# Performance work log

Measured on AMD Instinct MI355X. Metric: run time of the kernel, lower is better.

Reference implementation:

```python
import math
import jax, jax.numpy as jnp
import numpy as np

DIM = 2048
NUM_HEADS = 32
NUM_KV_HEADS = 8
HEAD_DIM = DIM // NUM_HEADS
KV_REPEAT = NUM_HEADS // NUM_KV_HEADS
BSZ, SEQ = 2, 2048
THRESHOLD = 0.05


def ternarize_ste(w):
    # scale = mean(|w|), clamped; ternary in {-1,0,1}; STE: fwd value is ternary,
    # grad flows straight through to w.
    scale = jnp.maximum(jnp.abs(w).mean(), 1e-6)
    ternary = jnp.where(w > THRESHOLD * scale, 1.0,
                        jnp.where(w < -THRESHOLD * scale, -1.0, 0.0)).astype(w.dtype)
    return w + jax.lax.stop_gradient(ternary - w)


def setup_inputs() -> dict:
    key = jax.random.key(0)
    kx, kq, kk, kv, ko = jax.random.split(key, 5)
    # kaiming_uniform_(a=sqrt(5)) => U(-b, b) with b = 1/sqrt(in_features)
    bound = 1.0 / math.sqrt(DIM)
    return {
        "x": jax.random.normal(kx, (BSZ, SEQ, DIM), dtype=jnp.float32),
        "wq": jax.random.uniform(kq, (DIM, DIM), jnp.float32, -bound, bound),
        "wk": jax.random.uniform(kk, (HEAD_DIM * NUM_KV_HEADS, DIM), jnp.float32, -bound, bound),
        "wv": jax.random.uniform(kv, (HEAD_DIM * NUM_KV_HEADS, DIM), jnp.float32, -bound, bound),
        "wo": jax.random.uniform(ko, (DIM, DIM), jnp.float32, -bound, bound),
    }


def reference(x, wq, wk, wv, wo):
    bsz, seq, _ = x.shape
    # BitLinear projections with ternarized weights (F.linear: x @ W^T)
    q = x @ ternarize_ste(wq).T                      # [b, s, dim]
    k = x @ ternarize_ste(wk).T                      # [b, s, kvh*hd]
    v = x @ ternarize_ste(wv).T

    q = q.reshape(bsz, seq, NUM_HEADS, HEAD_DIM)     # [b, s, H, d]
    k = k.reshape(bsz, seq, NUM_KV_HEADS, HEAD_DIM)
    v = v.reshape(bsz, seq, NUM_KV_HEADS, HEAD_DIM)
    # repeat_interleave over the kv-head axis to match query heads
    k = jnp.repeat(k, KV_REPEAT, axis=2)             # [b, s, H, d]
    v = jnp.repeat(v, KV_REPEAT, axis=2)

    scale = 1.0 / math.sqrt(HEAD_DIM)
    att = jnp.einsum('bqhd,bkhd->bhqk', q, k) * scale  # [b, H, s, s]
    causal = jnp.tril(jnp.ones((seq, seq), dtype=bool))
    att = jnp.where(causal, att, -jnp.inf)
    probs = jax.nn.softmax(att, axis=-1)
    out = jnp.einsum('bhqk,bkhd->bqhd', probs, v).reshape(bsz, seq, DIM)
    return out @ ternarize_ste(wo).T
```

## Files before the change

### kernel.cpp

```cpp
#include <hip/hip_runtime.h>

typedef _Float16 f16;
typedef f16  f16x8 __attribute__((ext_vector_type(8)));
typedef f16  f16x4 __attribute__((ext_vector_type(4)));
typedef float f32x4 __attribute__((ext_vector_type(4)));

#define DIM_   2048
#define SEQ_   2048
#define BATCH_ 2
#define MROWS_ (BATCH_*SEQ_)
#define HD_    64
#define KVW_   512

__device__ __forceinline__ f32x4 mfma16(f16x8 a, f16x8 b, f32x4 c) {
  return __builtin_amdgcn_mfma_f32_16x16x32_f16(a, b, c, 0, 0, 0);
}

typedef const __attribute__((address_space(1))) void gas_void;
typedef __attribute__((address_space(3))) void las_void;
__device__ __forceinline__ void gload16(const void* g, void* l) {
  __builtin_amdgcn_global_load_lds((gas_void*)g, (las_void*)l, 16, 0, 0);
}

__device__ __forceinline__ unsigned long long pk4(float a, float b, float c, float d) {
  union { _Float16 h[4]; unsigned long long u; } z;
  auto p0 = __builtin_amdgcn_cvt_pkrtz(a, b);
  auto p1 = __builtin_amdgcn_cvt_pkrtz(c, d);
  z.h[0] = p0[0]; z.h[1] = p0[1]; z.h[2] = p1[0]; z.h[3] = p1[1];
  return z.u;
}

__global__ __launch_bounds__(256)
void prep1(const float* __restrict__ x,
           const float* __restrict__ w0, const float* __restrict__ w1,
           const float* __restrict__ w2, const float* __restrict__ w3,
           float* __restrict__ parts, f16* __restrict__ hi, f16* __restrict__ lo) {
  const int id = blockIdx.y;
  if (id < 4) {
    const float* w = id == 0 ? w0 : id == 1 ? w1 : id == 2 ? w2 : w3;
    const int n4 = (id == 1 || id == 2) ? (KVW_ * DIM_ / 4) : (DIM_ * DIM_ / 4);
    float s = 0.f;
    for (int i = blockIdx.x * 256 + threadIdx.x; i < n4; i += gridDim.x * 256) {
      float4 v = *(const float4*)(w + (long)i * 4);
      s += fabsf(v.x) + fabsf(v.y) + fabsf(v.z) + fabsf(v.w);
    }
    #pragma unroll
    for (int off = 32; off > 0; off >>= 1)
      s += __shfl_down(s, off, 64);
    __shared__ float red[4];
    int lane = threadIdx.x & 63, wv = threadIdx.x >> 6;
    if (lane == 0) red[wv] = s;
    __syncthreads();
    if (threadIdx.x == 0)
      parts[id * 192 + blockIdx.x] = (red[0] + red[1]) + (red[2] + red[3]);
  } else {
    const int half = (MROWS_ * DIM_ / 4) / 2;
    const long base = (long)(id - 4) * half;
    for (int i = blockIdx.x * 256 + threadIdx.x; i < half; i += gridDim.x * 256) {
      float4 v = *(const float4*)(x + (base + i) * 4);
      f16x4 h, l;
      h[0] = (f16)v.x; l[0] = (f16)(v.x - (float)h[0]);
      h[1] = (f16)v.y; l[1] = (f16)(v.y - (float)h[1]);
      h[2] = (f16)v.z; l[2] = (f16)(v.z - (float)h[2]);
      h[3] = (f16)v.w; l[3] = (f16)(v.w - (float)h[3]);
      *(f16x4*)(hi + (base + i) * 4) = h;
      *(f16x4*)(lo + (base + i) * 4) = l;
    }
  }
}

__global__ __launch_bounds__(256)
void ternarize4(const float* __restrict__ w0, const float* __restrict__ w1,
                const float* __restrict__ w2, const float* __restrict__ w3,
                unsigned short* __restrict__ t0, unsigned short* __restrict__ t1,
                unsigned short* __restrict__ t2, unsigned short* __restrict__ t3,
                const float* __restrict__ parts) {
  const int id = blockIdx.y;
  const float* w = id == 0 ? w0 : id == 1 ? w1 : id == 2 ? w2 : w3;
  unsigned short* t = id == 0 ? t0 : id == 1 ? t1 : id == 2 ? t2 : t3;
  const int n = (id == 1 || id == 2) ? (KVW_ * DIM_) : (DIM_ * DIM_);

  __shared__ float thr_s;
  if (threadIdx.x < 64) {
    const int lane = threadIdx.x;
    float s = parts[id * 192 + lane] + parts[id * 192 + 64 + lane]
            + parts[id * 192 + 128 + lane];
    #pragma unroll
    for (int off = 32; off > 0; off >>= 1)
      s += __shfl_down(s, off, 64);
    if (lane == 0) thr_s = 0.05f * fmaxf(s / (float)n, 1e-6f);
  }
  __syncthreads();
  const float thr = thr_s;

  const int n4 = n >> 2;
  for (int i = blockIdx.x * 256 + threadIdx.x; i < n4; i += gridDim.x * 256) {
    float4 v = *(const float4*)(w + (long)i * 4);
    ushort4 o;
    o.x = v.x > thr ? 0x3C00 : (v.x < -thr ? 0xBC00 : 0);
    o.y = v.y > thr ? 0x3C00 : (v.y < -thr ? 0xBC00 : 0);
    o.z = v.z > thr ? 0x3C00 : (v.z < -thr ? 0xBC00 : 0);
    o.w = v.w > thr ? 0x3C00 : (v.w < -thr ? 0xBC00 : 0);
    *(ushort4*)(t + (long)i * 4) = o;
  }
}

__global__ __launch_bounds__(256, 2)
void gemm_qkv(const f16* __restrict__ Ah, const f16* __restrict__ Al,
              const f16* __restrict__ Bw,
              f16* __restrict__ O1, f16* __restrict__ O2,
              f16* __restrict__ K1, f16* __restrict__ K2,
              f16* __restrict__ OV) {
  constexpr int BUFSZ = 32768;
  __shared__ __attribute__((aligned(16))) char smem[2 * BUFSZ];

  const int id2 = (blockIdx.x & 7) * 48 + (blockIdx.x >> 3);
  const int bx  = id2 % 12;
  const int by  = id2 / 12;
  const int brow = by * 128;
  const int bcol = bx * 256;

  const int tid  = threadIdx.x;
  const int lane = tid & 63;
  const int wv   = tid >> 6;
  const int wr   = (wv >> 1) * 64;
  const int wc   = (wv & 1) * 128;
  const int fr   = lane & 15;
  const int fq   = lane >> 4;

  const bool lo_on = bcol < 2560;

  const int rl  = lane >> 2;
  const int scg = ((lane & 3) ^ ((lane >> 3) & 3)) * 8;
  const f16* gA0 = Ah + (long)(brow + wv * 32 + rl) * DIM_ + scg;
  const f16* gL0 = Al + (long)(brow + wv * 32 + rl) * DIM_ + scg;
  const f16* gB0 = Bw + (long)(bcol + wv * 64 + rl) * DIM_ + scg;
  const int wvbA = __builtin_amdgcn_readfirstlane(wv * 1024);
  const int wvbB = __builtin_amdgcn_readfirstlane(wv * 2048);

  auto STAGE = [&](int kt, int buf) {
    const int k0 = kt * 32;
    char* base = smem + buf * BUFSZ;
    f16* lA = (f16*)base + wvbA;
    f16* lL = (f16*)(base + 8192) + wvbA;
    f16* lB = (f16*)(base + 16384) + wvbB;
    gload16(gA0 + k0, lA);
    gload16(gA0 + k0 + 16 * DIM_, lA + 512);
    gload16(gB0 + k0, lB);
    gload16(gB0 + k0 + 16 * DIM_, lB + 512);
    gload16(gB0 + k0 + 32 * DIM_, lB + 1024);
    gload16(gB0 + k0 + 48 * DIM_, lB + 1536);
    if (lo_on) {
      gload16(gL0 + k0, lL);
      gload16(gL0 + k0 + 16 * DIM_, lL + 512);
    }
  };

  const int xga = (fq ^ ((fr >> 1) & 3)) * 8;

  f32x4 acc[4][8] = {};
  const int nk = DIM_ / 32;

  STAGE(0, 0);
  #pragma unroll 1
  for (int kt = 0; kt < nk; ++kt) {
    asm volatile("s_waitcnt vmcnt(0)" ::: "memory");
    __syncthreads();
    if (kt + 1 < nk) STAGE(kt + 1, (kt + 1) & 1);

    const char* base = smem + (kt & 1) * BUFSZ;
    const f16* cAh = (const f16*)base;
    const f16* cAl = (const f16*)(base + 8192);
    const f16* cB  = (const f16*)(base + 16384);

    f16x8 bfr[8];
    #pragma unroll
    for (int ni = 0; ni < 8; ++ni)
      bfr[ni] = *(const f16x8*)(cB + (wc + ni * 16 + fr) * 32 + xga);
    #pragma unroll
    for (int mi = 0; mi < 4; ++mi) {
      const int aoff = (wr + mi * 16 + fr) * 32 + xga;
      f16x8 ah = *(const f16x8*)(cAh + aoff);
      #pragma unroll
      for (int ni = 0; ni < 8; ++ni)
        acc[mi][ni] = mfma16(ah, bfr[ni], acc[mi][ni]);
      if (lo_on) {
        f16x8 al = *(const f16x8*)(cAl + aoff);
        #pragma unroll
        for (int ni = 0; ni < 8; ++ni)
          acc[mi][ni] = mfma16(al, bfr[ni], acc[mi][ni]);
      }
    }
  }

  const int colbase = bcol + wc;
  if (colbase < 2048) {
    #pragma unroll
    for (int mi = 0; mi < 4; ++mi)
      #pragma unroll
      for (int ni = 0; ni < 8; ++ni)
        #pragma unroll
        for (int r = 0; r < 4; ++r) {
          long idx = (long)(brow + wr + mi * 16 + fq * 4 + r) * DIM_
                   + colbase + ni * 16 + fr;
          float v = acc[mi][ni][r];
          f16 hv = (f16)v;
          O1[idx] = hv;
          O2[idx] = (f16)(v - (float)hv);
        }
  } else if (colbase < 2560) {
    #pragma unroll
    for (int mi = 0; mi < 4; ++mi)
      #pragma unroll
      for (int ni = 0; ni < 8; ++ni)
        #pragma unroll
        for (int r = 0; r < 4; ++r) {
          long idx = (long)(brow + wr + mi * 16 + fq * 4 + r) * KVW_
                   + (colbase - 2048) + ni * 16 + fr;
          float v = acc[mi][ni][r];
          f16 hv = (f16)v;
          K1[idx] = hv;
          K2[idx] = (f16)(v - (float)hv);
        }
  } else {
    f16* st = (f16*)smem + wv * 32 * 72;
    const int bb = brow >> 11;
    const int s0 = (brow & (SEQ_ - 1)) + wr;
    #pragma unroll
    for (int nh = 0; nh < 4; ++nh) {
      const int khh = ((colbase - 2560) >> 6) + (nh >> 1);
      const int db  = (nh & 1) * 32;
      #pragma unroll
      for (int nj = 0; nj < 2; ++nj) {
        const int ni = nh * 2 + nj;
        #pragma unroll
        for (int mi = 0; mi < 4; ++mi)
          #pragma unroll
          for (int r = 0; r < 4; ++r)
            st[(nj * 16 + fr) * 72 + mi * 16 + fq * 4 + r] = (f16)acc[mi][ni][r];
      }
      #pragma unroll
      for (int i = 0; i < 4; ++i) {
        int dl = i * 8 + (lane >> 3);
        f16x8 v = *(const f16x8*)(st + dl * 72 + (lane & 7) * 8);
        *(f16x8*)(OV + ((long)(bb * 8 + khh) * 64 + db + dl) * SEQ_
                  + s0 + (lane & 7) * 8) = v;
      }
    }
  }
}

__global__ __launch_bounds__(256)
void gemm_o(const f16* __restrict__ A, const f16* __restrict__ Bw,
            float* __restrict__ C) {
  constexpr int BUFSZ = 16384;
  __shared__ __attribute__((aligned(16))) char smem[2 * BUFSZ];

  const int cpx = gridDim.x >> 3;
  const int id2 = (blockIdx.x & 7) * cpx + (blockIdx.x >> 3);
  const int nbx = DIM_ >> 7;
  const int bx  = id2 % nbx;
  const int by  = id2 / nbx;
  const int brow = by * 128;
  const int bcol = bx * 128;

  const int tid  = threadIdx.x;
  const int lane = tid & 63;
  const int wv   = tid >> 6;
  const int wr   = (wv >> 1) * 64;
  const int wc   = (wv & 1) * 64;
  const int fr   = lane & 15;
  const int fq   = lane >> 4;

  const int srw = wv * 32 + (lane >> 2);
  const int scg = ((lane & 3) ^ ((lane >> 3) & 3)) * 8;
  const f16* gA0 = A + (long)(brow + srw) * DIM_ + scg;
  const f16* gA1 = gA0 + 16 * (long)DIM_;
  const f16* gB0 = Bw + (long)(bcol + srw) * DIM_ + scg;
  const f16* gB1 = gB0 + 16 * (long)DIM_;
  const int wvb = __builtin_amdgcn_readfirstlane(wv * 1024);

  auto STAGE = [&](int kt, int buf) {
    const int k0 = kt * 32;
    char* base = smem + buf * BUFSZ;
    f16* lA = (f16*)base + wvb;
    f16* lB = (f16*)(base + 8192) + wvb;
    gload16(gA0 + k0, lA);
    gload16(gA1 + k0, lA + 512);
    gload16(gB0 + k0, lB);
    gload16(gB1 + k0, lB + 512);
  };

  const int xga = (fq ^ ((fr >> 1) & 3)) * 8;

  f32x4 acc[4][4] = {};
  const int nk = DIM_ >> 5;

  STAGE(0, 0);
  #pragma unroll 1
  for (int kt = 0; kt < nk; ++kt) {
    asm volatile("s_waitcnt vmcnt(0)" ::: "memory");
    __syncthreads();
    if (kt + 1 < nk) STAGE(kt + 1, (kt + 1) & 1);

    const char* base = smem + (kt & 1) * BUFSZ;
    const f16* cA = (const f16*)base;
    const f16* cB = (const f16*)(base + 8192);

    f16x8 bfr[4];
    #pragma unroll
    for (int ni = 0; ni < 4; ++ni)
      bfr[ni] = *(const f16x8*)(cB + (wc + ni * 16 + fr) * 32 + xga);
    #pragma unroll
    for (int mi = 0; mi < 4; ++mi) {
      f16x8 ah = *(const f16x8*)(cA + (wr + mi * 16 + fr) * 32 + xga);
      #pragma unroll
      for (int ni = 0; ni < 4; ++ni)
        acc[mi][ni] = mfma16(ah, bfr[ni], acc[mi][ni]);
    }
  }

  #pragma unroll
  for (int mi = 0; mi < 4; ++mi)
    #pragma unroll
    for (int ni = 0; ni < 4; ++ni)
      #pragma unroll
      for (int r = 0; r < 4; ++r)
        C[(long)(brow + wr + mi * 16 + fq * 4 + r) * DIM_ + (bcol + wc + ni * 16 + fr)]
            = acc[mi][ni][r];
}

__global__ __launch_bounds__(256, 2)
void attn_kernel(const f16* __restrict__ qhi, const f16* __restrict__ qlo,
                 const f16* __restrict__ khi, const f16* __restrict__ klo,
                 const f16* __restrict__ vt,  f16* __restrict__ AO) {
  const int id2  = (blockIdx.x & 7) * 64 + (blockIdx.x >> 3);
  const int pr   = id2 & 31;
  const int cmb  = id2 >> 5;
  const int kh   = cmb & 7;
  const int b    = cmb >> 3;
  const int tid  = threadIdx.x;
  const int lane = tid & 63;
  const int w    = tid >> 6;
  const int fr   = lane & 15;
  const int fq   = lane >> 4;
  const int h    = kh * 4 + w;
  const int xr   = (fr & 7) << 4;

  __shared__ __attribute__((aligned(16))) char sKh[2][64 * 128];
  __shared__ __attribute__((aligned(16))) char sKl[2][64 * 128];
  __shared__ __attribute__((aligned(16))) char sVt[2][64 * 128];
  __shared__ __attribute__((aligned(16))) char sP [4][2][16 * 128];

  const int srow = w * 16 + (lane >> 3);
  const int scol = ((lane & 7) ^ (lane >> 3)) * 8;
  const f16* gK0 = khi + ((long)(b * SEQ_) + srow) * KVW_ + kh * HD_ + scol;
  const f16* gL0 = klo + ((long)(b * SEQ_) + srow) * KVW_ + kh * HD_ + scol;
  const f16* gV0 = vt + ((long)(b * 8 + kh) * HD_ + srow) * SEQ_ + scol;
  const int ldso = __builtin_amdgcn_readfirstlane(w * 2048);

  auto STAGE = [&](int kb, int buf) {
    const long ko = (long)kb * 64 * KVW_;
    const long vo = (long)kb * 64;
    gload16(gK0 + ko,             (char*)sKh[buf] + ldso);
    gload16(gK0 + ko + 8 * KVW_,  (char*)sKh[buf] + ldso + 1024);
    gload16(gL0 + ko,             (char*)sKl[buf] + ldso);
    gload16(gL0 + ko + 8 * KVW_,  (char*)sKl[buf] + ldso + 1024);
    gload16(gV0 + vo,             (char*)sVt[buf] + ldso);
    gload16(gV0 + vo + 8 * SEQ_,  (char*)sVt[buf] + ldso + 1024);
  };

  char* pw0 = sP[w][0];
  char* pw1 = sP[w][1];
  const float ce = 0.125f * 1.44269504f;

  #pragma unroll 1
  for (int pass = 0; pass < 2; ++pass) {
    const int t     = pass ? (63 - pr) : pr;
    const int nkv   = (t >> 1) + 1;
    const int qrow0 = t * 32;

    f16x8 qh[2][2], ql[2][2];
    #pragma unroll
    for (int st = 0; st < 2; ++st)
      #pragma unroll
      for (int ks = 0; ks < 2; ++ks) {
        const long qoff = (long)(b * SEQ_ + qrow0 + st * 16 + fr) * DIM_
                        + h * HD_ + ks * 32 + fq * 8;
        qh[st][ks] = *(const f16x8*)(qhi + qoff);
        ql[st][ks] = *(const f16x8*)(qlo + qoff);
      }

    __syncthreads();
    STAGE(0, 0);

    float m0 = -1e30f, m1 = -1e30f, l0 = 0.f, l1 = 0.f;
    f32x4 o0[4] = {}, o1[4] = {};
    int c = 0;

    #pragma unroll 1
    for (int kb = 0; kb < nkv; ++kb) {
      asm volatile("s_waitcnt vmcnt(0)" ::: "memory");
      __syncthreads();
      if (kb + 1 < nkv) STAGE(kb + 1, c ^ 1);
      const char* bK = sKh[c]; const char* bL = sKl[c]; const char* bV = sVt[c];

      f32x4 s0[4] = {}, s1[4] = {};
      __builtin_amdgcn_s_setprio(1);
      #pragma unroll
      for (int ks = 0; ks < 2; ++ks)
        #pragma unroll
        for (int ni = 0; ni < 4; ++ni) {
          const int rb = (ni * 16 + fr) * 128 + ((ks * 64 + fq * 16) ^ xr);
          f16x8 ah = *(const f16x8*)(bK + rb);
          f16x8 af = *(const f16x8*)(bL + rb);
          s0[ni] = mfma16(ah, qh[0][ks], s0[ni]);
          s0[ni] = mfma16(ah, ql[0][ks], s0[ni]);
          s0[ni] = mfma16(af, qh[0][ks], s0[ni]);
          s1[ni] = mfma16(ah, qh[1][ks], s1[ni]);
          s1[ni] = mfma16(ah, ql[1][ks], s1[ni]);
          s1[ni] = mfma16(af, qh[1][ks], s1[ni]);
        }
      __builtin_amdgcn_s_setprio(0);
      if (kb == nkv - 1) {
        #pragma unroll
        for (int ni = 0; ni < 4; ++ni)
          #pragma unroll
          for (int r = 0; r < 4; ++r) {
            const int kk = ni * 16 + fq * 4 + r;
            if (kk > (t & 1) * 32 + fr)      s0[ni][r] = -1e30f;
            if (kk > (t & 1) * 32 + 16 + fr) s1[ni][r] = -1e30f;
          }
      }

      #pragma unroll
      for (int st = 0; st < 2; ++st) {
        f32x4* s = st ? s1 : s0;
        float& m = st ? m1 : m0;
        float& l = st ? l1 : l0;
        f32x4* o = st ? o1 : o0;
        char* pw = st ? pw1 : pw0;

        float ma = fmaxf(fmaxf(s[0][0], s[0][1]), fmaxf(s[0][2], s[0][3]));
        float mb2 = fmaxf(fmaxf(s[1][0], s[1][1]), fmaxf(s[1][2], s[1][3]));
        float mc = fmaxf(fmaxf(s[2][0], s[2][1]), fmaxf(s[2][2], s[2][3]));
        float md = fmaxf(fmaxf(s[3][0], s[3][1]), fmaxf(s[3][2], s[3][3]));
        float mb = fmaxf(fmaxf(ma, mb2), fmaxf(mc, md));
        mb = fmaxf(mb, __shfl_xor(mb, 16, 64));
        mb = fmaxf(mb, __shfl_xor(mb, 32, 64));

        const float mo = m;
        const bool trig = mb > mo + 64.f;
        const float mn = trig ? mb : mo;
        m = mn;
        const float al = exp2f((mo - mn) * ce);
        const float tt = mn * ce;

        float rs = 0.f;
        #pragma unroll
        for (int ni = 0; ni < 4; ++ni) {
          #pragma unroll
          for (int r = 0; r < 4; ++r) {
            float pv = exp2f(fmaf(s[ni][r], ce, -tt));
            s[ni][r] = pv;
            rs += pv;
          }
          *(unsigned long long*)(pw + ((fr * 128 + ni * 32 + fq * 8) ^ xr)) =
              pk4(s[ni][0], s[ni][1], s[ni][2], s[ni][3]);
        }
        rs += __shfl_xor(rs, 16, 64);
        rs += __shfl_xor(rs, 32, 64);
        l = l * al + rs;

        if (__any(trig)) {
          #pragma unroll
          for (int r = 0; r < 4; ++r) {
            float alr = __shfl(al, ((lane >> 4) << 2) + r, 64);
            o[0][r] *= alr; o[1][r] *= alr; o[2][r] *= alr; o[3][r] *= alr;
          }
        }
      }

      __builtin_amdgcn_s_setprio(1);
      #pragma unroll
      for (int ks = 0; ks < 2; ++ks) {
        const int pb = (fr * 128 + ks * 64 + fq * 16) ^ xr;
        f16x8 pa0 = *(const f16x8*)(pw0 + pb);
        f16x8 pa1 = *(const f16x8*)(pw1 + pb);
        #pragma unroll
        for (int di = 0; di < 4; ++di) {
          f16x8 vf = *(const f16x8*)(bV + (di * 16 + fr) * 128
                                     + ((ks * 64 + fq * 16) ^ xr));
          o0[di] = mfma16(pa0, vf, o0[di]);
          o1[di] = mfma16(pa1, vf, o1[di]);
        }
      }
      __builtin_amdgcn_s_setprio(0);
      c ^= 1;
    }

    #pragma unroll
    for (int st = 0; st < 2; ++st) {
      const f32x4* o = st ? o1 : o0;
      const float l = st ? l1 : l0;
      float linv[4];
      #pragma unroll
      for (int r = 0; r < 4; ++r)
        linv[r] = 1.f / __shfl(l, ((lane >> 4) << 2) + r, 64);
      #pragma unroll
      for (int di = 0; di < 4; ++di)
        #pragma unroll
        for (int r = 0; r < 4; ++r)
          AO[(long)(b * SEQ_ + qrow0 + st * 16 + fq * 4 + r) * DIM_
             + h * HD_ + di * 16 + fr] = (f16)(o[di][r] * linv[r]);
    }
  }
}

extern "C" void kernel_launch(void* const* d_in, const int* in_sizes, int n_in,
                              void* d_out, int out_size, void* d_ws, size_t ws_size,
                              hipStream_t stream) {
  const float* x  = (const float*)d_in[0];
  const float* wq = (const float*)d_in[1];
  const float* wk = (const float*)d_in[2];
  const float* wv = (const float*)d_in[3];
  const float* wo = (const float*)d_in[4];
  char* ws = (char*)d_ws;

  size_t off = 0;
  float* parts = (float*)ws;                off = 4096;
  f16* x_hi  = (f16*)(ws + off);            off += (size_t)MROWS_ * DIM_ * 2;
  f16* x_lo  = (f16*)(ws + off);            off += (size_t)MROWS_ * DIM_ * 2;
  f16* wq_t  = (f16*)(ws + off);            off += (size_t)DIM_ * DIM_ * 2;
  f16* wkv_t = (f16*)(ws + off);            off += (size_t)1024 * DIM_ * 2;
  f16* wo_t  = (f16*)(ws + off);            off += (size_t)DIM_ * DIM_ * 2;
  f16* qhi   = (f16*)(ws + off);            off += (size_t)MROWS_ * DIM_ * 2;
  f16* qlo   = (f16*)(ws + off);            off += (size_t)MROWS_ * DIM_ * 2;
  f16* khi   = (f16*)(ws + off);            off += (size_t)MROWS_ * KVW_ * 2;
  f16* klo   = (f16*)(ws + off);            off += (size_t)MROWS_ * KVW_ * 2;
  f16* vtb   = (f16*)(ws + off);            off += (size_t)BATCH_ * 8 * 64 * SEQ_ * 2;
  f16* ao    = (f16*)(ws + off);            off += (size_t)MROWS_ * DIM_ * 2;

  prep1<<<dim3(192, 6), dim3(256), 0, stream>>>(x, wq, wk, wv, wo,
                                                parts, x_hi, x_lo);
  ternarize4<<<dim3(192, 4), dim3(256), 0, stream>>>(
      wq, wk, wv, wo,
      (unsigned short*)wq_t, (unsigned short*)wkv_t,
      (unsigned short*)(wkv_t + (size_t)KVW_ * DIM_), (unsigned short*)wo_t,
      parts);

  gemm_qkv<<<dim3(384), dim3(256), 0, stream>>>(
      x_hi, x_lo, wq_t, qhi, qlo, khi, klo, vtb);

  attn_kernel<<<dim3(32 * 8 * BATCH_), dim3(256), 0, stream>>>(
      qhi, qlo, khi, klo, vtb, ao);

  gemm_o<<<dim3((DIM_ / 128) * (MROWS_ / 128)), dim3(256), 0, stream>>>(
      ao, wo_t, (float*)d_out);
}
```

Before: 284.6 us.

## Single-buffer K tiles in attention to fit three blocks per CU

```diff
diff --git a/kernel.cpp b/kernel.cpp
--- a/kernel.cpp
+++ b/kernel.cpp
@@ -330,7 +330,7 @@
             = acc[mi][ni][r];
 }
 
-__global__ __launch_bounds__(256, 2)
+__global__ __launch_bounds__(256, 3)
 void attn_kernel(const f16* __restrict__ qhi, const f16* __restrict__ qlo,
                  const f16* __restrict__ khi, const f16* __restrict__ klo,
                  const f16* __restrict__ vt,  f16* __restrict__ AO) {
@@ -347,8 +347,8 @@
   const int h    = kh * 4 + w;
   const int xr   = (fr & 7) << 4;
 
-  __shared__ __attribute__((aligned(16))) char sKh[2][64 * 128];
-  __shared__ __attribute__((aligned(16))) char sKl[2][64 * 128];
+  __shared__ __attribute__((aligned(16))) char sKh[64 * 128];
+  __shared__ __attribute__((aligned(16))) char sKl[64 * 128];
   __shared__ __attribute__((aligned(16))) char sVt[2][64 * 128];
   __shared__ __attribute__((aligned(16))) char sP [4][2][16 * 128];
 
@@ -359,15 +359,17 @@
   const f16* gV0 = vt + ((long)(b * 8 + kh) * HD_ + srow) * SEQ_ + scol;
   const int ldso = __builtin_amdgcn_readfirstlane(w * 2048);
 
-  auto STAGE = [&](int kb, int buf) {
+  auto STAGE_K = [&](int kb) {
     const long ko = (long)kb * 64 * KVW_;
+    gload16(gK0 + ko,            sKh + ldso);
+    gload16(gK0 + ko + 8 * KVW_, sKh + ldso + 1024);
+    gload16(gL0 + ko,            sKl + ldso);
+    gload16(gL0 + ko + 8 * KVW_, sKl + ldso + 1024);
+  };
+  auto STAGE_V = [&](int kb, int buf) {
     const long vo = (long)kb * 64;
-    gload16(gK0 + ko,             (char*)sKh[buf] + ldso);
-    gload16(gK0 + ko + 8 * KVW_,  (char*)sKh[buf] + ldso + 1024);
-    gload16(gL0 + ko,             (char*)sKl[buf] + ldso);
-    gload16(gL0 + ko + 8 * KVW_,  (char*)sKl[buf] + ldso + 1024);
-    gload16(gV0 + vo,             (char*)sVt[buf] + ldso);
-    gload16(gV0 + vo + 8 * SEQ_,  (char*)sVt[buf] + ldso + 1024);
+    gload16(gV0 + vo,            (char*)sVt[buf] + ldso);
+    gload16(gV0 + vo + 8 * SEQ_, (char*)sVt[buf] + ldso + 1024);
   };
 
   char* pw0 = sP[w][0];
@@ -392,18 +394,18 @@
       }
 
     __syncthreads();
-    STAGE(0, 0);
+    STAGE_K(0);
+    STAGE_V(0, 0);
 
     float m0 = -1e30f, m1 = -1e30f, l0 = 0.f, l1 = 0.f;
     f32x4 o0[4] = {}, o1[4] = {};
-    int c = 0;
 
     #pragma unroll 1
     for (int kb = 0; kb < nkv; ++kb) {
       asm volatile("s_waitcnt vmcnt(0)" ::: "memory");
       __syncthreads();
-      if (kb + 1 < nkv) STAGE(kb + 1, c ^ 1);
-      const char* bK = sKh[c]; const char* bL = sKl[c]; const char* bV = sVt[c];
+      if (kb + 1 < nkv) STAGE_V(kb + 1, (kb + 1) & 1);
+      const char* bV = sVt[kb & 1];
 
       f32x4 s0[4] = {}, s1[4] = {};
       __builtin_amdgcn_s_setprio(1);
@@ -412,8 +414,8 @@
         #pragma unroll
         for (int ni = 0; ni < 4; ++ni) {
           const int rb = (ni * 16 + fr) * 128 + ((ks * 64 + fq * 16) ^ xr);
-          f16x8 ah = *(const f16x8*)(bK + rb);
-          f16x8 af = *(const f16x8*)(bL + rb);
+          f16x8 ah = *(const f16x8*)(sKh + rb);
+          f16x8 af = *(const f16x8*)(sKl + rb);
           s0[ni] = mfma16(ah, qh[0][ks], s0[ni]);
           s0[ni] = mfma16(ah, ql[0][ks], s0[ni]);
           s0[ni] = mfma16(af, qh[0][ks], s0[ni]);
@@ -422,6 +424,10 @@
           s1[ni] = mfma16(af, qh[1][ks], s1[ni]);
         }
       __builtin_amdgcn_s_setprio(0);
+
+      __syncthreads();
+      if (kb + 1 < nkv) STAGE_K(kb + 1);
+
       if (kb == nkv - 1) {
         #pragma unroll
         for (int ni = 0; ni < 4; ++ni)
@@ -496,7 +502,6 @@
         }
       }
       __builtin_amdgcn_s_setprio(0);
-      c ^= 1;
     }
 
     #pragma unroll
```

New measurement: 284.7 us. No clear change (+0.0%).
